# Kernel tuning notes

Measured on AMD Instinct MI355X. Metric: run time of the kernel, lower is better.

## Reference

```python
import jax, jax.numpy as jnp
import numpy as np

B, C, H, W = 16, 64, 32, 32
N_TOTAL = C * H * W          # 65536 flattened spatial units
N = 8192                     # samples_per_batch
EPS = 1e-12


def setup_inputs() -> dict:
    key = jax.random.key(0)
    k1, k2, k3 = jax.random.split(key, 3)
    layer_feature = jax.random.normal(k1, (B, C, H, W), dtype=jnp.float32)
    coordinates = jax.random.normal(k2, (N_TOTAL, 2), dtype=jnp.float32)
    # stand-in for torch.randperm(CHW)[:N]: unique in-range indices
    sampled_indices = jax.random.permutation(k3, N_TOTAL)[:N].astype(jnp.int64)
    return {"layer_feature": layer_feature, "coordinates": coordinates,
            "sampled_indices": sampled_indices}


def _masked_pearson(a, b, mask):
    # Pearson correlation between the masked (strict lower-triangle) entries
    cnt = jnp.sum(mask.astype(a.dtype))
    am = jnp.sum(jnp.where(mask, a, 0.0)) / cnt
    bm = jnp.sum(jnp.where(mask, b, 0.0)) / cnt
    ac = jnp.where(mask, a - am, 0.0)
    bc = jnp.where(mask, b - bm, 0.0)
    return jnp.sum(ac * bc) / (jnp.sqrt(jnp.sum(ac * ac)) * jnp.sqrt(jnp.sum(bc * bc)))


def reference(layer_feature, coordinates, sampled_indices):
    b = layer_feature.shape[0]
    feature = layer_feature.reshape(b, -1)[:, sampled_indices]   # [B, N]
    coords = coordinates[sampled_indices]                         # [N, 2]
    n = feature.shape[1]

    # distance similarity: 1 / (pdist + 1), full NxN (lower tri used)
    sq_norm = jnp.sum(coords * coords, axis=1)                    # [N]
    sq = sq_norm[:, None] + sq_norm[None, :] - 2.0 * (coords @ coords.T)
    sq = jnp.maximum(sq, 0.0)
    dist = jnp.sqrt(jnp.where(sq > EPS, sq, EPS))                 # safe sqrt
    distance_similarity = 1.0 / (dist + 1.0)                      # [N, N]

    # response similarity: corrcoef of feature.T -> NxN correlation over B
    X = feature.T                                                 # [N, B]
    Xc = X - jnp.mean(X, axis=1, keepdims=True)
    Xn = Xc / jnp.sqrt(jnp.sum(Xc * Xc, axis=1, keepdims=True))
    response_similarity = Xn @ Xn.T                               # [N, N]

    mask = jnp.tril(jnp.ones((n, n), dtype=bool), k=-1)           # strict lower tri
    similarity_alignment = _masked_pearson(response_similarity,
                                           distance_similarity, mask)
    return (1.0 - similarity_alignment) / 2.0
```

## Files before the change

kernel.cpp:

```cpp
#include <hip/hip_runtime.h>
#include <hip/hip_bf16.h>
#include <math.h>

#define NSAMP 8192
#define BATCH 16
#define CHW   65536
#define EPS_F 1e-12f

#define BT    128
#define NBT   (NSAMP / BT)
#define NINT  (NBT * (NBT - 1) / 2)
#define NBLK  (NINT + NBT)

typedef __attribute__((ext_vector_type(8))) short short8v;
typedef __attribute__((ext_vector_type(4))) float f32x4;

#define OFF_XA 86016
#define OFF_C2 (OFF_XA + NSAMP * 32 * 2)

__global__ void __launch_bounds__(256)
prep_kernel(const float* __restrict__ feat, const float* __restrict__ coords,
            const int* __restrict__ sidx,
            __hip_bfloat16* __restrict__ XA, float* __restrict__ C2) {
    int t = blockIdx.x * 256 + threadIdx.x;
    int n = t >> 4, b = t & 15;
    int id = sidx[n];
    float v = feat[b * CHW + id];

    float m = v;
    m += __shfl_xor(m, 1, 16); m += __shfl_xor(m, 2, 16);
    m += __shfl_xor(m, 4, 16); m += __shfl_xor(m, 8, 16);
    float c = v - m * (1.0f / 16.0f);
    float q = c * c;
    q += __shfl_xor(q, 1, 16); q += __shfl_xor(q, 2, 16);
    q += __shfl_xor(q, 4, 16); q += __shfl_xor(q, 8, 16);
    float x = c * (1.0f / sqrtf(q));

    __hip_bfloat16 hi = __float2bfloat16(x);
    float hif = __bfloat162float(hi);
    __hip_bfloat16 lo = __float2bfloat16(x - hif);

    XA[n * 32 + b]      = hi;
    XA[n * 32 + 16 + b] = lo;
    if (b == 0) {
        float2 cc = reinterpret_cast<const float2*>(coords)[id];
        reinterpret_cast<float2*>(C2)[n] = cc;
    }
}

template<bool DIAG>
__global__ void __launch_bounds__(256)
pair_kernel(const __hip_bfloat16* __restrict__ XA,
            const float* __restrict__ C2,
            double* __restrict__ partials) {
    int bi, bj, slot;
    if (DIAG) {
        bi = bj = blockIdx.x; slot = NINT + blockIdx.x;
    } else {
        int t = blockIdx.x;
        int e = (int)((1.0f + sqrtf(1.0f + 8.0f * (float)t)) * 0.5f);
        while (e * (e - 1) / 2 > t) --e;
        while ((e + 1) * e / 2 <= t) ++e;
        bi = e; bj = t - e * (e - 1) / 2; slot = t;
    }
    const int tid = threadIdx.x;
    const int wid = tid >> 6, l = tid & 63;
    const int wi = wid >> 1, wj = wid & 1;
    const int col = l & 15, kg = l >> 4, rb = kg * 4;

    const int iW = bi * BT + wi * 64;
    const int jW = bj * BT + wj * 64;

    float fSa = 0, fSb = 0, fSab = 0, fSaa = 0, fSbb = 0;

    if (!(DIAG && wj > wi)) {
        const short* XAs = reinterpret_cast<const short*>(XA);

        short8v afr[4];
        float cix[4][4], ciy[4][4];
#pragma unroll
        for (int ti = 0; ti < 4; ++ti) {
            int rowA = iW + ti * 16 + col;
            afr[ti] = *reinterpret_cast<const short8v*>(XAs + rowA * 32 + kg * 8);
            const float4* cp =
                reinterpret_cast<const float4*>(C2 + (iW + ti * 16 + rb) * 2);
            float4 ca = cp[0], cb = cp[1];
            cix[ti][0] = ca.x; ciy[ti][0] = ca.y;
            cix[ti][1] = ca.z; ciy[ti][1] = ca.w;
            cix[ti][2] = cb.x; ciy[ti][2] = cb.y;
            cix[ti][3] = cb.z; ciy[ti][3] = cb.w;
        }
#pragma unroll
        for (int tj = 0; tj < 4; ++tj) {
            int rowB = jW + tj * 16 + col;
            short8v bhl = *reinterpret_cast<const short8v*>(XAs + rowB * 32 + kg * 8);
            short8v blh = *reinterpret_cast<const short8v*>(XAs + rowB * 32 + ((kg ^ 2) * 8));
            int gj = jW + tj * 16 + col;
            float2 cj = reinterpret_cast<const float2*>(C2)[gj];
#pragma unroll
            for (int ti = 0; ti < 4; ++ti) {
                if (DIAG && wi == wj && ti < tj) continue;
                f32x4 acc = {0.f, 0.f, 0.f, 0.f};
                acc = __builtin_amdgcn_mfma_f32_16x16x32_bf16(afr[ti], bhl, acc, 0, 0, 0);
                acc = __builtin_amdgcn_mfma_f32_16x16x32_bf16(afr[ti], blh, acc, 0, 0, 0);
                const int giB = iW + ti * 16 + rb;
#pragma unroll
                for (int r = 0; r < 4; ++r) {
                    float a  = acc[r];
                    float dx = cix[ti][r] - cj.x, dy = ciy[ti][r] - cj.y;
                    float s2 = fmaf(dx, dx, dy * dy);
                    s2 = fmaxf(s2, EPS_F);
                    float bb = __builtin_amdgcn_rcpf(sqrtf(s2) + 1.0f);
                    float am = a;
                    if (DIAG) {
                        bool mk = (giB + r) > gj;
                        bb = mk ? bb : 0.0f;
                        am = mk ? a  : 0.0f;
                    }
                    fSa += am;
                    fSb += bb;
                    fSab = fmaf(a,  bb, fSab);
                    fSaa = fmaf(am, am, fSaa);
                    fSbb = fmaf(bb, bb, fSbb);
                }
            }
        }
    }

    double dSa = fSa, dSb = fSb, dSab = fSab, dSaa = fSaa, dSbb = fSbb;
#pragma unroll
    for (int o = 32; o > 0; o >>= 1) {
        dSa  += __shfl_down(dSa,  o, 64);
        dSb  += __shfl_down(dSb,  o, 64);
        dSab += __shfl_down(dSab, o, 64);
        dSaa += __shfl_down(dSaa, o, 64);
        dSbb += __shfl_down(dSbb, o, 64);
    }
    __shared__ double red[4][5];
    if (l == 0) {
        red[wid][0] = dSa;  red[wid][1] = dSb;  red[wid][2] = dSab;
        red[wid][3] = dSaa; red[wid][4] = dSbb;
    }
    __syncthreads();
    if (tid == 0) {
#pragma unroll
        for (int q = 0; q < 5; ++q)
            partials[slot * 5 + q] =
                red[0][q] + red[1][q] + red[2][q] + red[3][q];
    }
}

__global__ void __launch_bounds__(256)
finish_kernel(const double* __restrict__ partials, float* __restrict__ out) {
    double s0 = 0, s1 = 0, s2 = 0, s3 = 0, s4 = 0;
    for (int b = threadIdx.x; b < NBLK; b += 256) {
        s0 += partials[b * 5 + 0]; s1 += partials[b * 5 + 1];
        s2 += partials[b * 5 + 2]; s3 += partials[b * 5 + 3];
        s4 += partials[b * 5 + 4];
    }
    const int lane = threadIdx.x & 63, wid = threadIdx.x >> 6;
#pragma unroll
    for (int o = 32; o > 0; o >>= 1) {
        s0 += __shfl_down(s0, o, 64); s1 += __shfl_down(s1, o, 64);
        s2 += __shfl_down(s2, o, 64); s3 += __shfl_down(s3, o, 64);
        s4 += __shfl_down(s4, o, 64);
    }
    __shared__ double red[4][5];
    if (lane == 0) {
        red[wid][0] = s0; red[wid][1] = s1; red[wid][2] = s2;
        red[wid][3] = s3; red[wid][4] = s4;
    }
    __syncthreads();
    if (threadIdx.x == 0) {
        double Sa  = red[0][0] + red[1][0] + red[2][0] + red[3][0];
        double Sb  = red[0][1] + red[1][1] + red[2][1] + red[3][1];
        double Sab = red[0][2] + red[1][2] + red[2][2] + red[3][2];
        double Saa = red[0][3] + red[1][3] + red[2][3] + red[3][3];
        double Sbb = red[0][4] + red[1][4] + red[2][4] + red[3][4];
        const double cnt = (double)NSAMP * (double)(NSAMP - 1) * 0.5;
        double am = Sa / cnt, bm = Sb / cnt;
        double cov = Sab - cnt * am * bm;
        double va  = Saa - cnt * am * am;
        double vb  = Sbb - cnt * bm * bm;
        double corr = cov / (sqrt(va) * sqrt(vb));
        out[0] = (float)((1.0 - corr) * 0.5);
    }
}

extern "C" void kernel_launch(void* const* d_in, const int* in_sizes, int n_in,
                              void* d_out, int out_size, void* d_ws, size_t ws_size,
                              hipStream_t stream) {
    const float* feat   = (const float*)d_in[0];
    const float* coords = (const float*)d_in[1];
    const int*   sidx   = (const int*)d_in[2];
    float* out = (float*)d_out;

    double* partials = (double*)d_ws;
    __hip_bfloat16* XA = (__hip_bfloat16*)((char*)d_ws + OFF_XA);
    float* C2 = (float*)((char*)d_ws + OFF_C2);

    prep_kernel<<<NSAMP * BATCH / 256, 256, 0, stream>>>(feat, coords, sidx,
                                                         XA, C2);
    pair_kernel<false><<<NINT, 256, 0, stream>>>(XA, C2, partials);
    pair_kernel<true><<<NBT, 256, 0, stream>>>(XA, C2, partials);
    finish_kernel<<<1, 256, 0, stream>>>(partials, out);
}
```

Measured before the change: 102.7 us.

## Merge diagonal, off-diagonal and finish kernels into one launch with last-block reduction

The separate off-diagonal and diagonal pair kernels are folded into one launch that picks its role from blockIdx. The final reduction now runs in the last block to finish, detected with an atomic counter that the prep kernel resets, so the finish kernel disappears. sqrtf is replaced with the hardware sqrt intrinsic. This cuts launch gaps and tail effects, at the cost of a global atomic and threadfence per block.

```diff
diff --git a/kernel.cpp b/kernel.cpp
--- a/kernel.cpp
+++ b/kernel.cpp
@@ -15,13 +15,16 @@
 typedef __attribute__((ext_vector_type(8))) short short8v;
 typedef __attribute__((ext_vector_type(4))) float f32x4;
 
-#define OFF_XA 86016
-#define OFF_C2 (OFF_XA + NSAMP * 32 * 2)
+#define OFF_CNT 83200
+#define OFF_XA  86016
+#define OFF_C2  (OFF_XA + NSAMP * 32 * 2)
 
 __global__ void __launch_bounds__(256)
 prep_kernel(const float* __restrict__ feat, const float* __restrict__ coords,
             const int* __restrict__ sidx,
-            __hip_bfloat16* __restrict__ XA, float* __restrict__ C2) {
+            __hip_bfloat16* __restrict__ XA, float* __restrict__ C2,
+            int* __restrict__ counter) {
+    if (blockIdx.x == 0 && threadIdx.x == 0) *counter = 0;
     int t = blockIdx.x * 256 + threadIdx.x;
     int n = t >> 4, b = t & 15;
     int id = sidx[n];
@@ -49,20 +52,79 @@
 }
 
 template<bool DIAG>
+__device__ __forceinline__ void
+compute_tiles(const short* __restrict__ XAs, const float* __restrict__ C2,
+              int iW, int jW, int wi, int wj, int col, int kg, int rb,
+              float& fSa, float& fSb, float& fSab, float& fSaa, float& fSbb) {
+    short8v afr[4];
+    float cix[4][4], ciy[4][4];
+#pragma unroll
+    for (int ti = 0; ti < 4; ++ti) {
+        int rowA = iW + ti * 16 + col;
+        afr[ti] = *reinterpret_cast<const short8v*>(XAs + rowA * 32 + kg * 8);
+        const float4* cp =
+            reinterpret_cast<const float4*>(C2 + (iW + ti * 16 + rb) * 2);
+        float4 ca = cp[0], cb = cp[1];
+        cix[ti][0] = ca.x; ciy[ti][0] = ca.y;
+        cix[ti][1] = ca.z; ciy[ti][1] = ca.w;
+        cix[ti][2] = cb.x; ciy[ti][2] = cb.y;
+        cix[ti][3] = cb.z; ciy[ti][3] = cb.w;
+    }
+#pragma unroll
+    for (int tj = 0; tj < 4; ++tj) {
+        int rowB = jW + tj * 16 + col;
+        short8v bhl = *reinterpret_cast<const short8v*>(XAs + rowB * 32 + kg * 8);
+        short8v blh = *reinterpret_cast<const short8v*>(XAs + rowB * 32 + ((kg ^ 2) * 8));
+        int gj = jW + tj * 16 + col;
+        float2 cj = reinterpret_cast<const float2*>(C2)[gj];
+#pragma unroll
+        for (int ti = 0; ti < 4; ++ti) {
+            if (DIAG && wi == wj && ti < tj) continue;
+            f32x4 acc = {0.f, 0.f, 0.f, 0.f};
+            acc = __builtin_amdgcn_mfma_f32_16x16x32_bf16(afr[ti], bhl, acc, 0, 0, 0);
+            acc = __builtin_amdgcn_mfma_f32_16x16x32_bf16(afr[ti], blh, acc, 0, 0, 0);
+            const int giB = iW + ti * 16 + rb;
+#pragma unroll
+            for (int r = 0; r < 4; ++r) {
+                float a  = acc[r];
+                float dx = cix[ti][r] - cj.x, dy = ciy[ti][r] - cj.y;
+                float s2 = fmaf(dx, dx, dy * dy);
+                s2 = fmaxf(s2, EPS_F);
+                float bb = __builtin_amdgcn_rcpf(
+                               __builtin_amdgcn_sqrtf(s2) + 1.0f);
+                float am = a;
+                if (DIAG) {
+                    bool mk = (giB + r) > gj;
+                    bb = mk ? bb : 0.0f;
+                    am = mk ? a  : 0.0f;
+                }
+                fSa += am;
+                fSb += bb;
+                fSab = fmaf(a,  bb, fSab);
+                fSaa = fmaf(am, am, fSaa);
+                fSbb = fmaf(bb, bb, fSbb);
+            }
+        }
+    }
+}
+
 __global__ void __launch_bounds__(256)
 pair_kernel(const __hip_bfloat16* __restrict__ XA,
             const float* __restrict__ C2,
-            double* __restrict__ partials) {
-    int bi, bj, slot;
-    if (DIAG) {
-        bi = bj = blockIdx.x; slot = NINT + blockIdx.x;
+            double* __restrict__ partials, int* __restrict__ counter,
+            float* __restrict__ out) {
+    const bool diag = (blockIdx.x >= NINT);
+    int bi, bj;
+    if (diag) {
+        bi = bj = blockIdx.x - NINT;
     } else {
         int t = blockIdx.x;
         int e = (int)((1.0f + sqrtf(1.0f + 8.0f * (float)t)) * 0.5f);
         while (e * (e - 1) / 2 > t) --e;
         while ((e + 1) * e / 2 <= t) ++e;
-        bi = e; bj = t - e * (e - 1) / 2; slot = t;
-    }
+        bi = e; bj = t - e * (e - 1) / 2;
+    }
+    const int slot = blockIdx.x;
     const int tid = threadIdx.x;
     const int wid = tid >> 6, l = tid & 63;
     const int wi = wid >> 1, wj = wid & 1;
@@ -72,59 +134,15 @@
     const int jW = bj * BT + wj * 64;
 
     float fSa = 0, fSb = 0, fSab = 0, fSaa = 0, fSbb = 0;
-
-    if (!(DIAG && wj > wi)) {
-        const short* XAs = reinterpret_cast<const short*>(XA);
-
-        short8v afr[4];
-        float cix[4][4], ciy[4][4];
-#pragma unroll
-        for (int ti = 0; ti < 4; ++ti) {
-            int rowA = iW + ti * 16 + col;
-            afr[ti] = *reinterpret_cast<const short8v*>(XAs + rowA * 32 + kg * 8);
-            const float4* cp =
-                reinterpret_cast<const float4*>(C2 + (iW + ti * 16 + rb) * 2);
-            float4 ca = cp[0], cb = cp[1];
-            cix[ti][0] = ca.x; ciy[ti][0] = ca.y;
-            cix[ti][1] = ca.z; ciy[ti][1] = ca.w;
-            cix[ti][2] = cb.x; ciy[ti][2] = cb.y;
-            cix[ti][3] = cb.z; ciy[ti][3] = cb.w;
-        }
-#pragma unroll
-        for (int tj = 0; tj < 4; ++tj) {
-            int rowB = jW + tj * 16 + col;
-            short8v bhl = *reinterpret_cast<const short8v*>(XAs + rowB * 32 + kg * 8);
-            short8v blh = *reinterpret_cast<const short8v*>(XAs + rowB * 32 + ((kg ^ 2) * 8));
-            int gj = jW + tj * 16 + col;
-            float2 cj = reinterpret_cast<const float2*>(C2)[gj];
-#pragma unroll
-            for (int ti = 0; ti < 4; ++ti) {
-                if (DIAG && wi == wj && ti < tj) continue;
-                f32x4 acc = {0.f, 0.f, 0.f, 0.f};
-                acc = __builtin_amdgcn_mfma_f32_16x16x32_bf16(afr[ti], bhl, acc, 0, 0, 0);
-                acc = __builtin_amdgcn_mfma_f32_16x16x32_bf16(afr[ti], blh, acc, 0, 0, 0);
-                const int giB = iW + ti * 16 + rb;
-#pragma unroll
-                for (int r = 0; r < 4; ++r) {
-                    float a  = acc[r];
-                    float dx = cix[ti][r] - cj.x, dy = ciy[ti][r] - cj.y;
-                    float s2 = fmaf(dx, dx, dy * dy);
-                    s2 = fmaxf(s2, EPS_F);
-                    float bb = __builtin_amdgcn_rcpf(sqrtf(s2) + 1.0f);
-                    float am = a;
-                    if (DIAG) {
-                        bool mk = (giB + r) > gj;
-                        bb = mk ? bb : 0.0f;
-                        am = mk ? a  : 0.0f;
-                    }
-                    fSa += am;
-                    fSb += bb;
-                    fSab = fmaf(a,  bb, fSab);
-                    fSaa = fmaf(am, am, fSaa);
-                    fSbb = fmaf(bb, bb, fSbb);
-                }
-            }
-        }
+    const short* XAs = reinterpret_cast<const short*>(XA);
+
+    if (diag) {
+        if (wj <= wi)
+            compute_tiles<true >(XAs, C2, iW, jW, wi, wj, col, kg, rb,
+                                 fSa, fSb, fSab, fSaa, fSbb);
+    } else {
+        compute_tiles<false>(XAs, C2, iW, jW, wi, wj, col, kg, rb,
+                             fSa, fSb, fSab, fSaa, fSbb);
     }
 
     double dSa = fSa, dSb = fSb, dSab = fSab, dSaa = fSaa, dSbb = fSbb;
@@ -137,6 +155,7 @@
         dSbb += __shfl_down(dSbb, o, 64);
     }
     __shared__ double red[4][5];
+    __shared__ int isLast;
     if (l == 0) {
         red[wid][0] = dSa;  red[wid][1] = dSb;  red[wid][2] = dSab;
         red[wid][3] = dSaa; red[wid][4] = dSbb;
@@ -147,31 +166,33 @@
         for (int q = 0; q < 5; ++q)
             partials[slot * 5 + q] =
                 red[0][q] + red[1][q] + red[2][q] + red[3][q];
-    }
-}
-
-__global__ void __launch_bounds__(256)
-finish_kernel(const double* __restrict__ partials, float* __restrict__ out) {
+        __threadfence();
+        int old = atomicAdd(counter, 1);
+        isLast = (old == NBLK - 1);
+    }
+    __syncthreads();
+
+    if (!isLast) return;
+    __threadfence();
     double s0 = 0, s1 = 0, s2 = 0, s3 = 0, s4 = 0;
-    for (int b = threadIdx.x; b < NBLK; b += 256) {
+    for (int b = tid; b < NBLK; b += 256) {
         s0 += partials[b * 5 + 0]; s1 += partials[b * 5 + 1];
         s2 += partials[b * 5 + 2]; s3 += partials[b * 5 + 3];
         s4 += partials[b * 5 + 4];
     }
-    const int lane = threadIdx.x & 63, wid = threadIdx.x >> 6;
 #pragma unroll
     for (int o = 32; o > 0; o >>= 1) {
         s0 += __shfl_down(s0, o, 64); s1 += __shfl_down(s1, o, 64);
         s2 += __shfl_down(s2, o, 64); s3 += __shfl_down(s3, o, 64);
         s4 += __shfl_down(s4, o, 64);
     }
-    __shared__ double red[4][5];
-    if (lane == 0) {
+    __syncthreads();
+    if (l == 0) {
         red[wid][0] = s0; red[wid][1] = s1; red[wid][2] = s2;
         red[wid][3] = s3; red[wid][4] = s4;
     }
     __syncthreads();
-    if (threadIdx.x == 0) {
+    if (tid == 0) {
         double Sa  = red[0][0] + red[1][0] + red[2][0] + red[3][0];
         double Sb  = red[0][1] + red[1][1] + red[2][1] + red[3][1];
         double Sab = red[0][2] + red[1][2] + red[2][2] + red[3][2];
@@ -196,12 +217,11 @@
     float* out = (float*)d_out;
 
     double* partials = (double*)d_ws;
+    int*    counter  = (int*)((char*)d_ws + OFF_CNT);
     __hip_bfloat16* XA = (__hip_bfloat16*)((char*)d_ws + OFF_XA);
     float* C2 = (float*)((char*)d_ws + OFF_C2);
 
     prep_kernel<<<NSAMP * BATCH / 256, 256, 0, stream>>>(feat, coords, sidx,
-                                                         XA, C2);
-    pair_kernel<false><<<NINT, 256, 0, stream>>>(XA, C2, partials);
-    pair_kernel<true><<<NBT, 256, 0, stream>>>(XA, C2, partials);
-    finish_kernel<<<1, 256, 0, stream>>>(partials, out);
-}
+                                                         XA, C2, counter);
+    pair_kernel<<<NBLK, 256, 0, stream>>>(XA, C2, partials, counter, out);
+}
```

Measured after the change: 110.8 us. 1.08x slower.
